# Optimization experiments

Measured on AMD Instinct MI355X. Metric: run time of the kernel, lower is better.

## Reference

```python
import jax, jax.numpy as jnp
import numpy as np

OUT = 7  # output_size of the ROI pool

def setup_inputs() -> dict:
    key = jax.random.key(0)
    # batched ROI crops: [N_rois, C, H, W] with H=W=14 (divisible by OUT=7,
    # so adaptive max-pool windows are exact non-overlapping 2x2 blocks)
    rois = jax.random.normal(key, (512, 256, 14, 14), dtype=jnp.float32)
    return {"rois": rois}

def reference(rois) -> jnp.ndarray:
    N, C, H, W = rois.shape
    kh, kw = H // OUT, W // OUT
    # AdaptiveMaxPool2d with H % OUT == 0 and W % OUT == 0 reduces to
    # max over non-overlapping (kh, kw) windows: start=floor(i*H/O)=i*kh,
    # end=ceil((i+1)*H/O)=(i+1)*kh, identical to the adaptive formula.
    x = rois.reshape(N, C, OUT, kh, OUT, kw)
    return x.max(axis=(3, 5))  # [N, C, OUT, OUT]
```

## Files before the change

kernel.cpp:

```cpp
#include <hip/hip_runtime.h>


typedef float f32x4 __attribute__((ext_vector_type(4)));

#define PPB   16
#define BLOCK 256

__global__ __launch_bounds__(BLOCK)
void ROIPooling_86466281603470_kernel(const float* __restrict__ in,
                                      float* __restrict__ out) {
    __shared__ float lds[PPB * 196];

    const int pb = blockIdx.x * PPB;

    const f32x4* __restrict__ in4 =
        reinterpret_cast<const f32x4*>(in + (size_t)pb * 196);
    f32x4* lds4 = reinterpret_cast<f32x4*>(lds);
    #pragma unroll
    for (int v = threadIdx.x; v < PPB * 49; v += BLOCK) {
        lds4[v] = in4[v];
    }
    __syncthreads();

    f32x4* __restrict__ out4 =
        reinterpret_cast<f32x4*>(out + (size_t)pb * 49);
    const int t = threadIdx.x;
    if (t < PPB * 49 / 4) {
        f32x4 r;
        #pragma unroll
        for (int q = 0; q < 4; ++q) {
            int o   = 4 * t + q;
            int p   = o / 49;
            int rem = o - p * 49;
            int i   = rem / 7;
            int j   = rem - i * 7;
            const float* base = lds + p * 196 + i * 28 + 2 * j;
            float2 a = *reinterpret_cast<const float2*>(base);
            float2 b = *reinterpret_cast<const float2*>(base + 14);
            r[q] = fmaxf(fmaxf(a.x, a.y), fmaxf(b.x, b.y));
        }
        out4[t] = r;
    }
}

extern "C" void kernel_launch(void* const* d_in, const int* in_sizes, int n_in,
                              void* d_out, int out_size, void* d_ws, size_t ws_size,
                              hipStream_t stream) {
    const float* in = (const float*)d_in[0];
    float* out = (float*)d_out;
    int n_planes = out_size / 49;
    int grid = n_planes / PPB;
    ROIPooling_86466281603470_kernel<<<grid, BLOCK, 0, stream>>>(in, out);
}
```

Baseline: 24.35 us.

## Load ROI planes directly into LDS per wavefront and drop block barrier

Each wavefront now owns four planes, fetches them with global_load_lds direct-to-LDS transfers, and waits on vmcnt instead of a block-wide __syncthreads. This removes the VGPR round trip for the staging copy and the cross-wave barrier. Correctness relies on the waitcnt covering LDS-write visibility for the async loads within a wave, which is fragile because the compiler may not track these builtin writes.

```diff
diff --git a/kernel.cpp b/kernel.cpp
--- a/kernel.cpp
+++ b/kernel.cpp
@@ -11,35 +11,44 @@
                                       float* __restrict__ out) {
     __shared__ float lds[PPB * 196];
 
-    const int pb = blockIdx.x * PPB;
+    const int lane = threadIdx.x & 63;
+    const int w    = threadIdx.x >> 6;
+    const size_t pb = (size_t)blockIdx.x * PPB;
 
-    const f32x4* __restrict__ in4 =
-        reinterpret_cast<const f32x4*>(in + (size_t)pb * 196);
-    f32x4* lds4 = reinterpret_cast<f32x4*>(lds);
+    const float* gbase = in + pb * 196 + w * 784;
+    float*       lbase = lds + w * 784;
+
     #pragma unroll
-    for (int v = threadIdx.x; v < PPB * 49; v += BLOCK) {
-        lds4[v] = in4[v];
+    for (int k = 0; k < 3; ++k) {
+        __builtin_amdgcn_global_load_lds(
+            (const __attribute__((address_space(1))) void*)(gbase + k * 256 + lane * 4),
+            (__attribute__((address_space(3))) void*)(lbase + k * 256),
+            16, 0, 0);
     }
-    __syncthreads();
+    if (lane < 4) {
+        __builtin_amdgcn_global_load_lds(
+            (const __attribute__((address_space(1))) void*)(gbase + 768 + lane * 4),
+            (__attribute__((address_space(3))) void*)(lbase + 768),
+            16, 0, 0);
+    }
+    asm volatile("s_waitcnt vmcnt(0)" ::: "memory");
 
-    f32x4* __restrict__ out4 =
-        reinterpret_cast<f32x4*>(out + (size_t)pb * 49);
-    const int t = threadIdx.x;
-    if (t < PPB * 49 / 4) {
+    if (lane < 49) {
         f32x4 r;
         #pragma unroll
         for (int q = 0; q < 4; ++q) {
-            int o   = 4 * t + q;
+            int o   = 4 * lane + q;
             int p   = o / 49;
             int rem = o - p * 49;
             int i   = rem / 7;
             int j   = rem - i * 7;
-            const float* base = lds + p * 196 + i * 28 + 2 * j;
+            const float* base = lbase + p * 196 + i * 28 + 2 * j;
             float2 a = *reinterpret_cast<const float2*>(base);
             float2 b = *reinterpret_cast<const float2*>(base + 14);
             r[q] = fmaxf(fmaxf(a.x, a.y), fmaxf(b.x, b.y));
         }
-        out4[t] = r;
+        f32x4* out4 = reinterpret_cast<f32x4*>(out + pb * 49 + w * 196);
+        out4[lane] = r;
     }
 }
 
```

Result: no change. 24.67 us (+1.3%).
